# Kernel tuning notes

Measured on AMD Instinct MI355X. Metric: run time of the kernel, lower is better.

The kernel has to match this reference:

```python
import jax, jax.numpy as jnp
import numpy as np

B, N, S, D2, K = 16, 4096, 512, 384, 5
BIG = 1e10
EPS = float(np.finfo(np.float32).eps)


def masked_bn(x, mask_f, gamma, beta):
    # x: [B, N, C]; mask_f: [B, N, 1] float. Training-mode batch norm over valid positions only.
    n = jnp.maximum(mask_f.sum(), 1.0)
    mean = (x * mask_f).sum(axis=(0, 1)) / n                       # [C]
    var = (jnp.square(x - mean) * mask_f).sum(axis=(0, 1)) / n     # [C]
    xh = (x - mean) * jax.lax.rsqrt(var + 1e-5)
    return (xh * gamma + beta) * mask_f


def setup_inputs() -> dict:
    key = jax.random.key(0)
    ks = jax.random.split(key, 10)
    xyz1 = jax.random.normal(ks[0], (B, N, 3), dtype=jnp.float32)
    xyz2 = jax.random.normal(ks[1], (B, S, 3), dtype=jnp.float32)
    points1 = jax.random.normal(ks[2], (B, N, 3), dtype=jnp.float32)
    points2 = jax.random.normal(ks[3], (B, S, D2), dtype=jnp.float32)
    point_lens = jax.random.randint(ks[4], (B,), N // 2, N + 1)
    embedding_lens = jax.random.randint(ks[5], (B,), S // 2, S + 1)
    point_mask = jnp.arange(N)[None, :] < point_lens[:, None]      # [B, N] bool
    W0 = jax.random.normal(ks[6], (D2, D2 + 3), dtype=jnp.float32) * 0.02
    W1 = jax.random.normal(ks[7], (D2, D2), dtype=jnp.float32) * 0.02
    return {
        "xyz1": xyz1, "xyz2": xyz2, "points1": points1, "points2": points2,
        "point_lens": point_lens, "embedding_lens": embedding_lens,
        "point_mask": point_mask,
        "W0": W0, "gamma0": jnp.ones((D2,), jnp.float32), "beta0": jnp.zeros((D2,), jnp.float32),
        "W1": W1, "gamma1": jnp.ones((D2,), jnp.float32), "beta1": jnp.zeros((D2,), jnp.float32),
    }


def reference(xyz1, xyz2, points1, points2, point_lens, embedding_lens, point_mask,
              W0, gamma0, beta0, W1, gamma1, beta1):
    # --- KNN (squared euclidean, ragged key lengths) ---
    diff = xyz1[:, :, None, :] - xyz2[:, None, :, :]               # [B, N, S, 3]
    d2 = jnp.sum(diff * diff, axis=-1)                             # [B, N, S]
    key_valid = jnp.arange(S)[None, :] < embedding_lens[:, None]   # [B, S]
    d2 = jnp.where(key_valid[:, None, :], d2, BIG)
    neg_d, idx = jax.lax.top_k(-d2, K)                             # [B, N, K]
    dists = -neg_d

    # --- inverse-distance weighted interpolation ---
    dist_recip = 1.0 / (dists + EPS)
    weight = dist_recip / dist_recip.sum(axis=2, keepdims=True)    # [B, N, K]
    gathered = jax.vmap(lambda p, i: p[i])(points2, idx)           # [B, N, K, D2]
    interpolated = (gathered * weight[..., None]).sum(axis=2)      # [B, N, D2]

    # --- concat coords + MLP (1x1 conv, masked BN, GELU) ---
    new_points = jnp.concatenate([points1, interpolated], axis=-1)  # [B, N, D2+3]
    mask_f = point_mask[..., None].astype(new_points.dtype)

    x = jnp.einsum('bnc,oc->bno', new_points, W0)
    x = masked_bn(x, mask_f, gamma0, beta0)
    x = jax.nn.gelu(x, approximate=False)
    x = jnp.einsum('bnc,oc->bno', x, W1)
    x = masked_bn(x, mask_f, gamma1, beta1)
    return x, idx
```

## Files before the change

### kernel.cpp

```cpp
#include <hip/hip_runtime.h>
#include <stdint.h>

typedef unsigned short u16;
typedef unsigned int u32;

#define B_ 16
#define N_ 4096
#define S_ 512
#define D2_ 384
#define K_ 5
#define CIN 387
#define KP 416
#define M_ (B_*N_)


typedef float f32x4 __attribute__((ext_vector_type(4)));
typedef u32 u32x4 __attribute__((ext_vector_type(4)));
typedef __bf16 bf16x8 __attribute__((ext_vector_type(8)));

__device__ __forceinline__ float bf2f(u16 h) {
  union { u32 u; float f; } v; v.u = ((u32)h) << 16; return v.f;
}
__device__ __forceinline__ u16 f2bf(float f) {
  union { float f; u32 u; } v; v.f = f;
  u32 u = v.u;
  u32 r = (u + 0x7FFFu + ((u >> 16) & 1u)) >> 16;
  return (u16)r;
}

__device__ __forceinline__ float erf_approx(float x) {
  float ax = fabsf(x);
  float t = __builtin_amdgcn_rcpf(fmaf(0.3275911f, ax, 1.0f));
  float p = fmaf(t, 1.061405429f, -1.453152027f);
  p = fmaf(p, t, 1.421413741f);
  p = fmaf(p, t, -0.284496736f);
  p = fmaf(p, t, 0.254829592f);
  p = p * t;
  float e = __expf(-ax * ax);
  float r = fmaf(-p, e, 1.0f);
  return copysignf(r, x);
}

__device__ __forceinline__ float gelu_f(float y) {
  return 0.5f * y * (1.f + erf_approx(y * 0.70710678118654752f));
}

__device__ __forceinline__ void gld16(const void* g, void* l) {
  __builtin_amdgcn_global_load_lds(
      (const __attribute__((address_space(1))) unsigned int*)g,
      (__attribute__((address_space(3))) unsigned int*)l, 16, 0, 0);
}

__global__ void prep_kernel(const float* __restrict__ W0, u16* __restrict__ W0p,
                            const float* __restrict__ W1, u16* __restrict__ W1c,
                            float* __restrict__ stats) {
  int bi = blockIdx.x;
  int tid = threadIdx.x;
  if (bi < 624) {
    int i = bi * 256 + tid;
    int r = i / KP, c = i - r * KP;
    float v = 0.f;
    if (c < 384)      v = W0[r * CIN + 3 + c];
    else if (c < CIN) v = W0[r * CIN + (c - 384)];
    W0p[i] = (c < CIN) ? f2bf(v) : (u16)0;
  } else if (bi < 1200) {
    int i = (bi - 624) * 256 + tid;
    W1c[i] = f2bf(W1[i]);
  } else {
    int i = (bi - 1200) * 256 + tid;
    if (i < 1536) stats[i] = 0.f;
  }
}

__global__ __launch_bounds__(256) void knn_kernel(
    const float* __restrict__ xyz1, const float* __restrict__ xyz2,
    const float* __restrict__ points1, const int* __restrict__ emb_lens,
    u16* __restrict__ A1, float* __restrict__ idx_out,
    float* __restrict__ wq, int* __restrict__ iq)
{
  __shared__ float4 sxyz[S_];
  __shared__ float sd[256][K_];
  __shared__ int   si[256][K_];

  int b = blockIdx.x >> 6;
  int n0 = (blockIdx.x & 63) << 6;
  int tid = threadIdx.x;

  const float* kb = xyz2 + (size_t)b * S_ * 3;
  for (int i = tid; i < S_; i += 256)
    sxyz[i] = make_float4(kb[3*i], kb[3*i+1], kb[3*i+2], 0.f);
  __syncthreads();

  int L = emb_lens[b];
  int q = tid & 63, chunk = tid >> 6;
  const float* qp = xyz1 + ((size_t)b * N_ + n0 + q) * 3;
  float qx = qp[0], qy = qp[1], qz = qp[2];

  float d0=3e38f, d1=3e38f, d2=3e38f, d3=3e38f, d4=3e38f;
  int   i0=0, i1=0, i2=0, i3=0, i4=0;
  int sbase = chunk << 7;

  #pragma unroll 4
  for (int t = 0; t < 128; ++t) {
    int s = sbase + t;
    float4 k4 = sxyz[s];
    float dx = __fsub_rn(qx, k4.x), dy = __fsub_rn(qy, k4.y), dz = __fsub_rn(qz, k4.z);
    float dd = __fadd_rn(__fadd_rn(__fmul_rn(dx,dx), __fmul_rn(dy,dy)),
                         __fmul_rn(dz,dz));
    if (s >= L) dd = 1e10f;

    bool c = dd < d4;
    d4 = c ? dd : d4; i4 = c ? s : i4;
    c = d4 < d3;
    { float tf = c ? d4 : d3; int ti = c ? i4 : i3;
      d4 = c ? d3 : d4;       i4 = c ? i3 : i4;
      d3 = tf;                i3 = ti; }
    c = d3 < d2;
    { float tf = c ? d3 : d2; int ti = c ? i3 : i2;
      d3 = c ? d2 : d3;       i3 = c ? i2 : i3;
      d2 = tf;                i2 = ti; }
    c = d2 < d1;
    { float tf = c ? d2 : d1; int ti = c ? i2 : i1;
      d2 = c ? d1 : d2;       i2 = c ? i1 : i2;
      d1 = tf;                i1 = ti; }
    c = d1 < d0;
    { float tf = c ? d1 : d0; int ti = c ? i1 : i0;
      d1 = c ? d0 : d1;       i1 = c ? i0 : i1;
      d0 = tf;                i0 = ti; }
  }
  sd[tid][0]=d0; sd[tid][1]=d1; sd[tid][2]=d2; sd[tid][3]=d3; sd[tid][4]=d4;
  si[tid][0]=i0; si[tid][1]=i1; si[tid][2]=i2; si[tid][3]=i3; si[tid][4]=i4;
  __syncthreads();

  if (tid < 64) {
    int p0 = 0, p1 = 0, p2 = 0, p3 = 0;
    float md[K_]; int mi[K_];
    #pragma unroll
    for (int k = 0; k < K_; ++k) {
      float a0 = sd[tid][p0],       a1 = sd[tid + 64][p1];
      float a2 = sd[tid + 128][p2], a3 = sd[tid + 192][p3];
      bool s01 = a1 < a0;
      bool s23 = a3 < a2;
      float m01 = s01 ? a1 : a0;
      float m23 = s23 ? a3 : a2;
      bool shi = m23 < m01;
      int r0 = s01 ? si[tid + 64][p1]  : si[tid][p0];
      int r1 = s23 ? si[tid + 192][p3] : si[tid + 128][p2];
      md[k] = shi ? m23 : m01;
      mi[k] = shi ? r1 : r0;
      p0 += (!shi && !s01); p1 += (!shi && s01);
      p2 += (shi && !s23);  p3 += (shi && s23);
    }
    float w[K_]; float ws = 0.f;
    #pragma unroll
    for (int k = 0; k < K_; ++k) { w[k] = 1.f / (md[k] + 1.1920929e-7f); ws += w[k]; }
    float inv = 1.f / ws;
    size_t row = (size_t)b * N_ + n0 + tid;
    #pragma unroll
    for (int k = 0; k < K_; ++k) {
      wq[row * K_ + k] = w[k] * inv;
      iq[row * K_ + k] = mi[k];
      idx_out[row * K_ + k] = (float)mi[k];
    }
    u16* rp = A1 + row * KP;
    const float* p1v = points1 + row * 3;
    rp[384] = f2bf(p1v[0]); rp[385] = f2bf(p1v[1]); rp[386] = f2bf(p1v[2]);
    #pragma unroll
    for (int c2 = CIN; c2 < KP; ++c2) rp[c2] = 0;
  }
}

__global__ __launch_bounds__(256) void interp_kernel(
    const float* __restrict__ points2,
    const float* __restrict__ wq, const int* __restrict__ iq,
    u16* __restrict__ A1)
{
  int lane = threadIdx.x & 63, wid = threadIdx.x >> 6;
  int i = blockIdx.x;
  int gq = ((i & 7) << 13) + ((i >> 3) << 2) + wid;
  int b = gq >> 12;

  float w[K_]; int id[K_];
  #pragma unroll
  for (int k = 0; k < K_; ++k) {
    w[k] = wq[(size_t)gq * K_ + k];
    id[k] = iq[(size_t)gq * K_ + k];
  }
  const float* p2 = points2 + (size_t)b * S_ * D2_;
  const float2* r0 = (const float2*)(p2 + (size_t)id[0] * D2_);
  const float2* r1 = (const float2*)(p2 + (size_t)id[1] * D2_);
  const float2* r2 = (const float2*)(p2 + (size_t)id[2] * D2_);
  const float2* r3 = (const float2*)(p2 + (size_t)id[3] * D2_);
  const float2* r4 = (const float2*)(p2 + (size_t)id[4] * D2_);
  u16* rp = A1 + (size_t)gq * KP;
  #pragma unroll
  for (int j = 0; j < 3; ++j) {
    int c2 = j * 64 + lane;
    float2 v0 = r0[c2], v1 = r1[c2], v2 = r2[c2], v3 = r3[c2], v4 = r4[c2];
    float a0 = w[0]*v0.x + w[1]*v1.x + w[2]*v2.x + w[3]*v3.x + w[4]*v4.x;
    float a1 = w[0]*v0.y + w[1]*v1.y + w[2]*v2.y + w[3]*v3.y + w[4]*v4.y;
    u32 pack = (u32)f2bf(a0) | ((u32)f2bf(a1) << 16);
    *(u32*)(rp + c2 * 2) = pack;
  }
}

template<bool F32OUT, int KT>
__global__ __launch_bounds__(256) void gemm_nt_kernel(
    const u16* __restrict__ A, int lda,
    const u16* __restrict__ W, int ldw,
    void* __restrict__ Cv, int ldc,
    const int* __restrict__ lens, float* __restrict__ sums)
{
  __shared__ __align__(16) u16 sA[2][128 * 32];
  __shared__ __align__(16) u16 sB[2][128 * 32];
  __shared__ float lsum[128], lsq[128];
  int tid = threadIdx.x;
  int lane = tid & 63, wid = tid >> 6;
  u32 bi = blockIdx.x;
  u32 s = bi >> 3;
  int m0 = (int)(((bi & 7) * 64 + s / 3) * 128);
  int n0 = (int)((s % 3) * 128);
  int wm = (wid & 1) * 64, wn = (wid >> 1) * 64;
  int frow = lane & 15, quad = lane >> 4;

  if (tid < 128) { lsum[tid] = 0.f; lsq[tid] = 0.f; }

  int grow = wid * 16 + (lane >> 2);
  int cq = (lane & 3) * 8;
  const u16* gA0 = A + (size_t)(m0 + grow) * lda + cq;
  const u16* gA1 = gA0 + (size_t)64 * lda;
  const u16* gB0 = W + (size_t)(n0 + grow) * ldw + cq;
  const u16* gB1 = gB0 + (size_t)64 * ldw;

  f32x4 acc[4][4];
  f32x4 zero4 = {0.f, 0.f, 0.f, 0.f};
  #pragma unroll
  for (int i = 0; i < 4; ++i)
    #pragma unroll
    for (int j = 0; j < 4; ++j) acc[i][j] = zero4;

  gld16(gA0, sA[0] + wid * 512); gld16(gA1, sA[0] + (wid + 4) * 512);
  gld16(gB0, sB[0] + wid * 512); gld16(gB1, sB[0] + (wid + 4) * 512);
  gA0 += 32; gA1 += 32; gB0 += 32; gB1 += 32;

  #pragma unroll
  for (int kt = 0; kt < KT; ++kt) {
    __syncthreads();
    int p = kt & 1;
    if (kt + 1 < KT) {
      int np = p ^ 1;
      gld16(gA0, sA[np] + wid * 512); gld16(gA1, sA[np] + (wid + 4) * 512);
      gld16(gB0, sB[np] + wid * 512); gld16(gB1, sB[np] + (wid + 4) * 512);
      gA0 += 32; gA1 += 32; gB0 += 32; gB1 += 32;
    }
    bf16x8 af[4], bfr[4];
    #pragma unroll
    for (int i = 0; i < 4; ++i)
      af[i] = *(const bf16x8*)(sA[p] + (wm + i * 16 + frow) * 32 + quad * 8);
    #pragma unroll
    for (int j = 0; j < 4; ++j)
      bfr[j] = *(const bf16x8*)(sB[p] + (wn + j * 16 + frow) * 32 + quad * 8);
    #pragma unroll
    for (int i = 0; i < 4; ++i)
      #pragma unroll
      for (int j = 0; j < 4; ++j)
        acc[i][j] = __builtin_amdgcn_mfma_f32_16x16x32_bf16(af[i], bfr[j], acc[i][j], 0, 0, 0);
  }

  int len = lens[m0 >> 12];
  float colS[4] = {0,0,0,0}, colQ[4] = {0,0,0,0};
  #pragma unroll
  for (int i = 0; i < 4; ++i) {
    #pragma unroll
    for (int j = 0; j < 4; ++j) {
      int col = n0 + wn + j * 16 + frow;
      #pragma unroll
      for (int r = 0; r < 4; ++r) {
        int m = m0 + wm + i * 16 + quad * 4 + r;
        float v = acc[i][j][r];
        if constexpr (F32OUT) ((float*)Cv)[(size_t)m * ldc + col] = v;
        else                  ((u16*)Cv)[(size_t)m * ldc + col] = f2bf(v);
        float x = ((m & 4095) < len) ? v : 0.f;
        colS[j] += x; colQ[j] += x * x;
      }
    }
  }
  #pragma unroll
  for (int j = 0; j < 4; ++j) {
    colS[j] += __shfl_xor(colS[j], 16); colS[j] += __shfl_xor(colS[j], 32);
    colQ[j] += __shfl_xor(colQ[j], 16); colQ[j] += __shfl_xor(colQ[j], 32);
    if (lane < 16) {
      int cl = wn + j * 16 + frow;
      atomicAdd(&lsum[cl], colS[j]);
      atomicAdd(&lsq[cl], colQ[j]);
    }
  }
  __syncthreads();
  if (tid < 128) {
    atomicAdd(&sums[n0 + tid], lsum[tid]);
    atomicAdd(&sums[384 + n0 + tid], lsq[tid]);
  }
}

__device__ __forceinline__ void finalize_to_lds(
    float* spar, const float* __restrict__ sums,
    const float* __restrict__ gamma, const float* __restrict__ beta,
    const int* __restrict__ lens, int tid)
{
  float nv = 0.f;
  #pragma unroll
  for (int b = 0; b < B_; ++b) nv += (float)lens[b];
  for (int c = tid; c < 384; c += 256) {
    float mean = sums[c] / nv;
    float var = sums[384 + c] / nv - mean * mean;
    var = fmaxf(var, 0.f);
    float rstd = rsqrtf(var + 1e-5f);
    float a = rstd * gamma[c];
    spar[c] = a;
    spar[384 + c] = beta[c] - mean * a;
  }
  __syncthreads();
}

__global__ __launch_bounds__(256) void apply_bn_gelu_kernel(
    u16* __restrict__ X, const float* __restrict__ sums,
    const float* __restrict__ gamma, const float* __restrict__ beta,
    const int* __restrict__ lens)
{
  __shared__ float spar[768];
  int tid = threadIdx.x;
  finalize_to_lds(spar, sums, gamma, beta, lens, tid);

  int t = blockIdx.x * 256 + tid;
  int half = t >= 196608;
  int tt = t - half * 196608;
  int r0 = tt / 48;
  int c0 = (tt - r0 * 48) * 8;
  float a[8], bb[8];
  #pragma unroll
  for (int j = 0; j < 8; ++j) { a[j] = spar[c0 + j]; bb[j] = spar[384 + c0 + j]; }

  const size_t rstride = (size_t)4096 * D2_;
  u16* base = X + (size_t)r0 * D2_ + c0 + (size_t)half * 8 * rstride;

  u32x4 v[8];
  #pragma unroll
  for (int it = 0; it < 8; ++it)
    v[it] = *(const u32x4*)(base + (size_t)it * rstride);
  #pragma unroll
  for (int it = 0; it < 8; ++it) {
    const u16* h = (const u16*)&v[it];
    u32x4 o; u16* ho = (u16*)&o;
    #pragma unroll
    for (int j = 0; j < 8; ++j) {
      float y = fmaf(bf2f(h[j]), a[j], bb[j]);
      ho[j] = f2bf(gelu_f(y));
    }
    *(u32x4*)(base + (size_t)it * rstride) = o;
  }
}

__global__ __launch_bounds__(256) void apply_bn_out_kernel(
    const u16* __restrict__ X, const float* __restrict__ sums,
    const float* __restrict__ gamma, const float* __restrict__ beta,
    const int* __restrict__ lens, float* __restrict__ out)
{
  __shared__ float spar[768];
  int tid = threadIdx.x;
  finalize_to_lds(spar, sums, gamma, beta, lens, tid);

  int t = blockIdx.x * 256 + tid;
  int half = t >= 196608;
  int tt = t - half * 196608;
  int r0 = tt / 48;
  int c0 = (tt - r0 * 48) * 8;
  float a[8], bb[8];
  #pragma unroll
  for (int j = 0; j < 8; ++j) { a[j] = spar[c0 + j]; bb[j] = spar[384 + c0 + j]; }

  const size_t rstride = (size_t)4096 * D2_;
  const u16* src = X + (size_t)r0 * D2_ + c0 + (size_t)half * 8 * rstride;
  float* dst = out + (size_t)r0 * D2_ + c0 + (size_t)half * 8 * rstride;

  u32x4 v[8];
  #pragma unroll
  for (int it = 0; it < 8; ++it)
    v[it] = *(const u32x4*)(src + (size_t)it * rstride);
  #pragma unroll
  for (int it = 0; it < 8; ++it) {
    int b = half * 8 + it;
    bool valid = r0 < lens[b];
    const u16* h = (const u16*)&v[it];
    f32x4 o0, o1;
    #pragma unroll
    for (int j = 0; j < 4; ++j) {
      float y = fmaf(bf2f(h[j]), a[j], bb[j]);
      o0[j] = valid ? y : 0.f;
    }
    #pragma unroll
    for (int j = 0; j < 4; ++j) {
      float y = fmaf(bf2f(h[4 + j]), a[4 + j], bb[4 + j]);
      o1[j] = valid ? y : 0.f;
    }
    float* op = dst + (size_t)it * rstride;
    __builtin_nontemporal_store(o0, (f32x4*)op);
    __builtin_nontemporal_store(o1, (f32x4*)(op + 4));
  }
}

extern "C" void kernel_launch(void* const* d_in, const int* in_sizes, int n_in,
                              void* d_out, int out_size, void* d_ws, size_t ws_size,
                              hipStream_t stream) {
  const float* xyz1    = (const float*)d_in[0];
  const float* xyz2    = (const float*)d_in[1];
  const float* points1 = (const float*)d_in[2];
  const float* points2 = (const float*)d_in[3];
  const int* point_lens = (const int*)d_in[4];
  const int* emb_lens   = (const int*)d_in[5];
  const float* W0 = (const float*)d_in[7];
  const float* g0 = (const float*)d_in[8];
  const float* b0 = (const float*)d_in[9];
  const float* W1 = (const float*)d_in[10];
  const float* g1 = (const float*)d_in[11];
  const float* b1 = (const float*)d_in[12];

  float* out = (float*)d_out;
  float* idx_out = out + (size_t)M_ * D2_;

  char* w = (char*)d_ws;
  u16* A1    = (u16*)w;
  u16* x1    = (u16*)w;
  u16* W0p   = (u16*)(w + 54525952);
  u16* W1c   = (u16*)(w + 54845440);
  u16* x0    = (u16*)(w + 55140352);
  float* wq  = (float*)(w + 55140352);
  int*   iq  = (int*)(w + 56451072);
  float* stats = (float*)(w + 105472000);

  prep_kernel<<<1206, 256, 0, stream>>>(W0, W0p, W1, W1c, stats);
  knn_kernel<<<1024, 256, 0, stream>>>(xyz1, xyz2, points1, emb_lens,
                                       A1, idx_out, wq, iq);
  interp_kernel<<<16384, 256, 0, stream>>>(points2, wq, iq, A1);
  gemm_nt_kernel<false, 13><<<1536, 256, 0, stream>>>(
      A1, KP, W0p, KP, x0, D2_, point_lens, stats);
  apply_bn_gelu_kernel<<<1536, 256, 0, stream>>>(x0, stats, g0, b0, point_lens);
  gemm_nt_kernel<false, 12><<<1536, 256, 0, stream>>>(
      x0, D2_, W1c, D2_, x1, D2_, point_lens, stats + 768);
  apply_bn_out_kernel<<<1536, 256, 0, stream>>>(x1, stats + 768, g1, b1,
                                                point_lens, out);
}
```

Measured before the change: 339.1 us.

## Load GEMM weight fragments directly to registers and triple-buffer A tiles

The GEMM no longer stages the weight (B) tile through shared memory. Each wave loads its B fragments straight from global memory into registers, prefetched one k-step ahead. The A tile gets a three-deep LDS ring with two stages in flight, and a raw s_barrier plus manual vmcnt waits replace __syncthreads. This is meant to cut LDS traffic and barrier stalls and deepen prefetch, but it leaves B reads uncoalesced and duplicated across waves. It also depends on hand-tuned waitcnt counts being correct for the async global-to-LDS loads.

```diff
diff --git a/kernel.cpp b/kernel.cpp
--- a/kernel.cpp
+++ b/kernel.cpp
@@ -211,8 +211,7 @@
     void* __restrict__ Cv, int ldc,
     const int* __restrict__ lens, float* __restrict__ sums)
 {
-  __shared__ __align__(16) u16 sA[2][128 * 32];
-  __shared__ __align__(16) u16 sB[2][128 * 32];
+  __shared__ __align__(16) u16 sA[3][128 * 32];
   __shared__ float lsum[128], lsq[128];
   int tid = threadIdx.x;
   int lane = tid & 63, wid = tid >> 6;
@@ -229,8 +228,8 @@
   int cq = (lane & 3) * 8;
   const u16* gA0 = A + (size_t)(m0 + grow) * lda + cq;
   const u16* gA1 = gA0 + (size_t)64 * lda;
-  const u16* gB0 = W + (size_t)(n0 + grow) * ldw + cq;
-  const u16* gB1 = gB0 + (size_t)64 * ldw;
+
+  const u16* gB = W + (size_t)(n0 + wn + frow) * ldw + quad * 8;
 
   f32x4 acc[4][4];
   f32x4 zero4 = {0.f, 0.f, 0.f, 0.f};
@@ -239,32 +238,44 @@
     #pragma unroll
     for (int j = 0; j < 4; ++j) acc[i][j] = zero4;
 
-  gld16(gA0, sA[0] + wid * 512); gld16(gA1, sA[0] + (wid + 4) * 512);
-  gld16(gB0, sB[0] + wid * 512); gld16(gB1, sB[0] + (wid + 4) * 512);
-  gA0 += 32; gA1 += 32; gB0 += 32; gB1 += 32;
+  auto stageA = [&](int buf) {
+    gld16(gA0, sA[buf] + wid * 512); gld16(gA1, sA[buf] + (wid + 4) * 512);
+    gA0 += 32; gA1 += 32;
+  };
+
+  stageA(0); stageA(1);
+  bf16x8 bfr[4];
+  #pragma unroll
+  for (int j = 0; j < 4; ++j)
+    bfr[j] = *(const bf16x8*)(gB + (size_t)(j * 16) * ldw);
+  asm volatile("s_waitcnt vmcnt(6)" ::: "memory");
 
   #pragma unroll
   for (int kt = 0; kt < KT; ++kt) {
-    __syncthreads();
-    int p = kt & 1;
+    __builtin_amdgcn_s_barrier();
+    __builtin_amdgcn_sched_barrier(0);
+    if (kt + 2 < KT) stageA((kt + 2) % 3);
+
+    bf16x8 af[4];
+    const u16* pA = sA[kt % 3];
+    #pragma unroll
+    for (int i = 0; i < 4; ++i)
+      af[i] = *(const bf16x8*)(pA + (wm + i * 16 + frow) * 32 + quad * 8);
+
+    bf16x8 bcur[4];
+    #pragma unroll
+    for (int j = 0; j < 4; ++j) bcur[j] = bfr[j];
     if (kt + 1 < KT) {
-      int np = p ^ 1;
-      gld16(gA0, sA[np] + wid * 512); gld16(gA1, sA[np] + (wid + 4) * 512);
-      gld16(gB0, sB[np] + wid * 512); gld16(gB1, sB[np] + (wid + 4) * 512);
-      gA0 += 32; gA1 += 32; gB0 += 32; gB1 += 32;
-    }
-    bf16x8 af[4], bfr[4];
-    #pragma unroll
-    for (int i = 0; i < 4; ++i)
-      af[i] = *(const bf16x8*)(sA[p] + (wm + i * 16 + frow) * 32 + quad * 8);
-    #pragma unroll
-    for (int j = 0; j < 4; ++j)
-      bfr[j] = *(const bf16x8*)(sB[p] + (wn + j * 16 + frow) * 32 + quad * 8);
+      #pragma unroll
+      for (int j = 0; j < 4; ++j)
+        bfr[j] = *(const bf16x8*)(gB + (size_t)(j * 16) * ldw + (kt + 1) * 32);
+    }
+
     #pragma unroll
     for (int i = 0; i < 4; ++i)
       #pragma unroll
       for (int j = 0; j < 4; ++j)
-        acc[i][j] = __builtin_amdgcn_mfma_f32_16x16x32_bf16(af[i], bfr[j], acc[i][j], 0, 0, 0);
+        acc[i][j] = __builtin_amdgcn_mfma_f32_16x16x32_bf16(af[i], bcur[j], acc[i][j], 0, 0, 0);
   }
 
   int len = lens[m0 >> 12];
```

New measurement: 341.7 us. Within noise of the previous version (+0.8%).
